# Optimization experiments

Hardware: AMD Instinct MI355X
Metric: run time of the kernel (lower is better)

The kernel has to match this reference:

```python
import jax, jax.numpy as jnp
import numpy as np

STATE_DIM = 4        # per-block state size (rel pos + rel vel, 2D)
N_NEIGH = 64         # neighbors per agent
BATCH = 4096         # observations in the batch (len(x) in torch code)
PHI_H, PHI_OUT = 256, 64
RHO_H, ACTION_DIM = 256, 2
R_AGENT = 0.15
A_MAX = 2.0


def setup_inputs() -> dict:
    key = jax.random.key(0)
    ks = jax.random.split(key, 5)

    def w(k, i, o):
        return jax.random.normal(k, (i, o), jnp.float32) / np.sqrt(i).astype(np.float32)

    x = jax.random.normal(ks[0], (BATCH, (N_NEIGH + 2) * STATE_DIM), jnp.float32)
    return dict(
        x=x,
        phi_w1=w(ks[1], STATE_DIM, PHI_H), phi_b1=jnp.zeros((PHI_H,), jnp.float32),
        phi_w2=w(ks[2], PHI_H, PHI_OUT), phi_b2=jnp.zeros((PHI_OUT,), jnp.float32),
        rho_w1=w(ks[3], PHI_OUT, RHO_H), rho_b1=jnp.zeros((RHO_H,), jnp.float32),
        rho_w2=w(ks[4], RHO_H, ACTION_DIM), rho_b2=jnp.zeros((ACTION_DIM,), jnp.float32),
    )


def reference(x, phi_w1, phi_b1, phi_w2, phi_b2, rho_w1, rho_b1, rho_w2, rho_b2):
    B = x.shape[0]
    blocks = x.reshape(B, -1, STATE_DIM)                 # [B, n_n+2, sd]
    # DeepSet: phi per block, permutation-invariant sum, rho head.
    h = jax.nn.relu(jnp.einsum('bns,sh->bnh', blocks, phi_w1) + phi_b1)
    phi = jnp.einsum('bnh,ho->bno', h, phi_w2) + phi_b2  # [B, n_n+2, phi_out]
    X = phi.sum(axis=1)                                  # [B, phi_out]
    h2 = jax.nn.relu(X @ rho_w1 + rho_b1)
    a = A_MAX * jnp.tanh(h2 @ rho_w2 + rho_b2)           # [B, action_dim]
    # Barrier: neighbor blocks start at block index 2; take first half (positions).
    p = blocks[:, 2:, : STATE_DIM // 2]                  # [B, n_n, 2]
    d = jnp.linalg.norm(p, axis=-1, keepdims=True)       # [B, n_n, 1]
    barrier = jnp.sum(-p / (d - R_AGENT) ** 2, axis=1)   # [B, 2]
    barrier = jax.lax.stop_gradient(barrier)  # torch goes through numpy -> detached
    a = a + barrier
    scale = A_MAX / jnp.max(a)  # torch.max(a_max)/torch.max(a_wbarrier), global max
    return jnp.where(scale < 1.0, a * scale, a)
```

## Files before the change

### kernel.cpp

```cpp
#include <hip/hip_runtime.h>
#include <math.h>


#define GROWS 4
#define NBLOCKS (4096 / GROWS)

__device__ __forceinline__ unsigned fkey(float f) {
    unsigned u = __float_as_uint(f);
    return (u & 0x80000000u) ? ~u : (u | 0x80000000u);
}
__device__ __forceinline__ float fkey_inv(unsigned k) {
    return __uint_as_float((k & 0x80000000u) ? (k & 0x7fffffffu) : ~k);
}
__device__ __forceinline__ float rlane(float v, int i) {
    return __uint_as_float(__builtin_amdgcn_readlane(__float_as_uint(v), i));
}

__global__ __launch_bounds__(256, 4) void barrier_net_main(
    const float* __restrict__ x,
    const float* __restrict__ w1,  const float* __restrict__ b1,
    const float* __restrict__ w2,  const float* __restrict__ b2,
    const float* __restrict__ rw1, const float* __restrict__ rb1,
    const float* __restrict__ rw2, const float* __restrict__ rb2,
    float* __restrict__ out, unsigned* __restrict__ maxkey)
{
    __shared__ float sH[GROWS][264];
    __shared__ float sXp[4][GROWS][68];
    __shared__ float sP4[4][GROWS][2];
    __shared__ float sbar[GROWS][2];
    __shared__ float sa[GROWS * 2];

    const int tid = threadIdx.x;
    const int ln  = tid & 63;
    const int wv  = tid >> 6;
    const int b0  = blockIdx.x * GROWS;
    const int row = __builtin_amdgcn_readfirstlane(b0 + wv);
    const float4* __restrict__ x4 = (const float4*)(x + (size_t)row * 264);

    float4 w1r0 = ((const float4*)(w1      ))[ln];
    float4 w1r1 = ((const float4*)(w1 + 256))[ln];
    float4 w1r2 = ((const float4*)(w1 + 512))[ln];
    float4 w1r3 = ((const float4*)(w1 + 768))[ln];
    float4 b1r  = ((const float4*)b1)[ln];
    float a0 = 0.f, a1 = 0.f, a2 = 0.f, a3 = 0.f;
    #pragma unroll 6
    for (int n = 0; n < 66; n++) {
        float4 xv = x4[n];
        float h0 = b1r.x, h1 = b1r.y, h2 = b1r.z, h3 = b1r.w;
        h0 = fmaf(xv.x, w1r0.x, h0); h1 = fmaf(xv.x, w1r0.y, h1);
        h2 = fmaf(xv.x, w1r0.z, h2); h3 = fmaf(xv.x, w1r0.w, h3);
        h0 = fmaf(xv.y, w1r1.x, h0); h1 = fmaf(xv.y, w1r1.y, h1);
        h2 = fmaf(xv.y, w1r1.z, h2); h3 = fmaf(xv.y, w1r1.w, h3);
        h0 = fmaf(xv.z, w1r2.x, h0); h1 = fmaf(xv.z, w1r2.y, h1);
        h2 = fmaf(xv.z, w1r2.z, h2); h3 = fmaf(xv.z, w1r2.w, h3);
        h0 = fmaf(xv.w, w1r3.x, h0); h1 = fmaf(xv.w, w1r3.y, h1);
        h2 = fmaf(xv.w, w1r3.z, h2); h3 = fmaf(xv.w, w1r3.w, h3);
        a0 += fmaxf(h0, 0.f); a1 += fmaxf(h1, 0.f);
        a2 += fmaxf(h2, 0.f); a3 += fmaxf(h3, 0.f);
    }
    ((float4*)sH[wv])[ln] = make_float4(a0, a1, a2, a3);

    {
        float4 pv = x4[ln + 2];
        float px = pv.x, py = pv.y;
        float d  = sqrtf(px * px + py * py);
        float t  = d - 0.15f;
        float inv = 1.0f / (t * t);
        float bx = -px * inv, by = -py * inv;
        #pragma unroll
        for (int m = 32; m >= 1; m >>= 1) {
            bx += __shfl_xor(bx, m);
            by += __shfl_xor(by, m);
        }
        if (ln == 0) { sbar[wv][0] = bx; sbar[wv][1] = by; }
    }
    __syncthreads();

    float Hq0 = sH[0][(wv << 6) + ln];
    float Hq1 = sH[1][(wv << 6) + ln];
    float Hq2 = sH[2][(wv << 6) + ln];
    float Hq3 = sH[3][(wv << 6) + ln];
    {
        float xp0 = 0.f, xp1 = 0.f, xp2 = 0.f, xp3 = 0.f;
        const float* w2q = w2 + (wv << 12);
        #pragma unroll 16
        for (int i = 0; i < 64; i++) {
            float wv2 = w2q[(i << 6) + ln];
            xp0 = fmaf(rlane(Hq0, i), wv2, xp0);
            xp1 = fmaf(rlane(Hq1, i), wv2, xp1);
            xp2 = fmaf(rlane(Hq2, i), wv2, xp2);
            xp3 = fmaf(rlane(Hq3, i), wv2, xp3);
        }
        sXp[wv][0][ln] = xp0; sXp[wv][1][ln] = xp1;
        sXp[wv][2][ln] = xp2; sXp[wv][3][ln] = xp3;
    }
    __syncthreads();

    float bb = 66.0f * b2[ln];
    float Xf0 = sXp[0][0][ln] + sXp[1][0][ln] + sXp[2][0][ln] + sXp[3][0][ln] + bb;
    float Xf1 = sXp[0][1][ln] + sXp[1][1][ln] + sXp[2][1][ln] + sXp[3][1][ln] + bb;
    float Xf2 = sXp[0][2][ln] + sXp[1][2][ln] + sXp[2][2][ln] + sXp[3][2][ln] + bb;
    float Xf3 = sXp[0][3][ln] + sXp[1][3][ln] + sXp[2][3][ln] + sXp[3][3][ln] + bb;

    float c0, c1, c2, c3;
    c0 = c1 = c2 = c3 = rb1[tid];
    #pragma unroll 16
    for (int i = 0; i < 64; i++) {
        float rwv = rw1[(i << 8) + tid];
        c0 = fmaf(rlane(Xf0, i), rwv, c0);
        c1 = fmaf(rlane(Xf1, i), rwv, c1);
        c2 = fmaf(rlane(Xf2, i), rwv, c2);
        c3 = fmaf(rlane(Xf3, i), rwv, c3);
    }
    c0 = fmaxf(c0, 0.f); c1 = fmaxf(c1, 0.f);
    c2 = fmaxf(c2, 0.f); c3 = fmaxf(c3, 0.f);

    {
        float2 r2 = ((const float2*)rw2)[tid];
        float p00 = c0 * r2.x, p01 = c0 * r2.y;
        float p10 = c1 * r2.x, p11 = c1 * r2.y;
        float p20 = c2 * r2.x, p21 = c2 * r2.y;
        float p30 = c3 * r2.x, p31 = c3 * r2.y;
        #pragma unroll
        for (int m = 32; m >= 1; m >>= 1) {
            p00 += __shfl_xor(p00, m); p01 += __shfl_xor(p01, m);
            p10 += __shfl_xor(p10, m); p11 += __shfl_xor(p11, m);
            p20 += __shfl_xor(p20, m); p21 += __shfl_xor(p21, m);
            p30 += __shfl_xor(p30, m); p31 += __shfl_xor(p31, m);
        }
        if (ln == 0) {
            sP4[wv][0][0] = p00; sP4[wv][0][1] = p01;
            sP4[wv][1][0] = p10; sP4[wv][1][1] = p11;
            sP4[wv][2][0] = p20; sP4[wv][2][1] = p21;
            sP4[wv][3][0] = p30; sP4[wv][3][1] = p31;
        }
    }
    __syncthreads();

    if (tid < GROWS * 2) {
        int r = tid >> 1, c = tid & 1;
        float pre = sP4[0][r][c] + sP4[1][r][c] + sP4[2][r][c] + sP4[3][r][c] + rb2[c];
        float a = 2.0f * tanhf(pre) + sbar[r][c];
        out[(b0 + r) * 2 + c] = a;
        sa[tid] = a;
    }
    __syncthreads();
    if (tid == 0) {
        float m = sa[0];
        #pragma unroll
        for (int i = 1; i < GROWS * 2; i++) m = fmaxf(m, sa[i]);
        atomicMax(maxkey, fkey(m));
    }
}

__global__ __launch_bounds__(256) void barrier_net_scale(
    float* __restrict__ out, const unsigned* __restrict__ maxkey)
{
    int i = blockIdx.x * 256 + threadIdx.x;
    float amax  = fkey_inv(*maxkey);
    float scale = 2.0f / amax;
    float a = out[i];
    out[i] = (scale < 1.0f) ? a * scale : a;
}

extern "C" void kernel_launch(void* const* d_in, const int* in_sizes, int n_in,
                              void* d_out, int out_size, void* d_ws, size_t ws_size,
                              hipStream_t stream) {
    const float* x   = (const float*)d_in[0];
    const float* w1  = (const float*)d_in[1];
    const float* b1  = (const float*)d_in[2];
    const float* w2  = (const float*)d_in[3];
    const float* b2  = (const float*)d_in[4];
    const float* rw1 = (const float*)d_in[5];
    const float* rb1 = (const float*)d_in[6];
    const float* rw2 = (const float*)d_in[7];
    const float* rb2 = (const float*)d_in[8];
    float* out = (float*)d_out;
    unsigned* maxkey = (unsigned*)d_ws;

    hipMemsetAsync(d_ws, 0, 4, stream);
    barrier_net_main<<<NBLOCKS, 256, 0, stream>>>(
        x, w1, b1, w2, b2, rw1, rb1, rw2, rb2, out, maxkey);
    barrier_net_scale<<<8192 / 256, 256, 0, stream>>>(out, maxkey);
}
```

Before: 98.68 us.

## Split fused DeepSet kernel into phase1 and phase234 with global H staging

Splits the single main kernel into two: the first computes the summed ReLU hidden activations and the barrier term per row and writes them to workspace, and the second runs the phi output layer and the rho MLP. The x row is now staged through shared memory instead of re-read per neighbor. The readlane broadcasts are replaced by float4 LDS reads. This trades an extra launch and a 4 MB global round-trip of H for simpler per-kernel register use and cheaper inner loops.

Result: slower. 104.1 us (+5.5%).

```diff
diff --git a/kernel.cpp b/kernel.cpp
--- a/kernel.cpp
+++ b/kernel.cpp
@@ -2,8 +2,7 @@
 #include <math.h>
 
 
-#define GROWS 4
-#define NBLOCKS (4096 / GROWS)
+#define NBLK 1024
 
 __device__ __forceinline__ unsigned fkey(float f) {
     unsigned u = __float_as_uint(f);
@@ -12,40 +11,35 @@
 __device__ __forceinline__ float fkey_inv(unsigned k) {
     return __uint_as_float((k & 0x80000000u) ? (k & 0x7fffffffu) : ~k);
 }
-__device__ __forceinline__ float rlane(float v, int i) {
-    return __uint_as_float(__builtin_amdgcn_readlane(__float_as_uint(v), i));
-}
-
-__global__ __launch_bounds__(256, 4) void barrier_net_main(
+
+__global__ __launch_bounds__(256, 4) void bn_phase1(
     const float* __restrict__ x,
-    const float* __restrict__ w1,  const float* __restrict__ b1,
-    const float* __restrict__ w2,  const float* __restrict__ b2,
-    const float* __restrict__ rw1, const float* __restrict__ rb1,
-    const float* __restrict__ rw2, const float* __restrict__ rb2,
-    float* __restrict__ out, unsigned* __restrict__ maxkey)
+    const float* __restrict__ w1, const float* __restrict__ b1,
+    float* __restrict__ H, float* __restrict__ bar)
 {
-    __shared__ float sH[GROWS][264];
-    __shared__ float sXp[4][GROWS][68];
-    __shared__ float sP4[4][GROWS][2];
-    __shared__ float sbar[GROWS][2];
-    __shared__ float sa[GROWS * 2];
+    __shared__ __align__(16) float sx[4][268];
 
     const int tid = threadIdx.x;
     const int ln  = tid & 63;
     const int wv  = tid >> 6;
-    const int b0  = blockIdx.x * GROWS;
-    const int row = __builtin_amdgcn_readfirstlane(b0 + wv);
+    const int row = blockIdx.x * 4 + wv;
     const float4* __restrict__ x4 = (const float4*)(x + (size_t)row * 264);
+
+    float4 xr = x4[ln];
+    float4 pv = x4[ln + 2];
+    ((float4*)sx[wv])[ln] = xr;
+    if (ln >= 62) ((float4*)sx[wv])[ln + 2] = pv;
 
     float4 w1r0 = ((const float4*)(w1      ))[ln];
     float4 w1r1 = ((const float4*)(w1 + 256))[ln];
     float4 w1r2 = ((const float4*)(w1 + 512))[ln];
     float4 w1r3 = ((const float4*)(w1 + 768))[ln];
     float4 b1r  = ((const float4*)b1)[ln];
+
     float a0 = 0.f, a1 = 0.f, a2 = 0.f, a3 = 0.f;
-    #pragma unroll 6
+    #pragma unroll 4
     for (int n = 0; n < 66; n++) {
-        float4 xv = x4[n];
+        float4 xv = ((const float4*)sx[wv])[n];
         float h0 = b1r.x, h1 = b1r.y, h2 = b1r.z, h3 = b1r.w;
         h0 = fmaf(xv.x, w1r0.x, h0); h1 = fmaf(xv.x, w1r0.y, h1);
         h2 = fmaf(xv.x, w1r0.z, h2); h3 = fmaf(xv.x, w1r0.w, h3);
@@ -58,10 +52,9 @@
         a0 += fmaxf(h0, 0.f); a1 += fmaxf(h1, 0.f);
         a2 += fmaxf(h2, 0.f); a3 += fmaxf(h3, 0.f);
     }
-    ((float4*)sH[wv])[ln] = make_float4(a0, a1, a2, a3);
-
-    {
-        float4 pv = x4[ln + 2];
+    ((float4*)(H + (size_t)row * 256))[ln] = make_float4(a0, a1, a2, a3);
+
+    {
         float px = pv.x, py = pv.y;
         float d  = sqrtf(px * px + py * py);
         float t  = d - 0.15f;
@@ -72,55 +65,96 @@
             bx += __shfl_xor(bx, m);
             by += __shfl_xor(by, m);
         }
-        if (ln == 0) { sbar[wv][0] = bx; sbar[wv][1] = by; }
-    }
-    __syncthreads();
-
-    float Hq0 = sH[0][(wv << 6) + ln];
-    float Hq1 = sH[1][(wv << 6) + ln];
-    float Hq2 = sH[2][(wv << 6) + ln];
-    float Hq3 = sH[3][(wv << 6) + ln];
+        if (ln == 0) { bar[row * 2 + 0] = bx; bar[row * 2 + 1] = by; }
+    }
+}
+
+__global__ __launch_bounds__(256, 4) void bn_phase234(
+    const float* __restrict__ H, const float* __restrict__ bar,
+    const float* __restrict__ w2,  const float* __restrict__ b2,
+    const float* __restrict__ rw1, const float* __restrict__ rb1,
+    const float* __restrict__ rw2, const float* __restrict__ rb2,
+    float* __restrict__ out, unsigned* __restrict__ wskey)
+{
+    __shared__ __align__(16) float sH[4][264];
+    __shared__ float sXp[4][4][68];
+    __shared__ __align__(16) float sX[4][68];
+    __shared__ float sP4[4][4][2];
+    __shared__ float sa[8];
+
+    const int tid = threadIdx.x;
+    const int ln  = tid & 63;
+    const int wv  = tid >> 6;
+    const int b0  = blockIdx.x * 4;
+
+    ((float4*)sH[wv])[ln] = ((const float4*)(H + (size_t)(b0 + wv) * 256))[ln];
+    __syncthreads();
+
     {
         float xp0 = 0.f, xp1 = 0.f, xp2 = 0.f, xp3 = 0.f;
         const float* w2q = w2 + (wv << 12);
-        #pragma unroll 16
-        for (int i = 0; i < 64; i++) {
-            float wv2 = w2q[(i << 6) + ln];
-            xp0 = fmaf(rlane(Hq0, i), wv2, xp0);
-            xp1 = fmaf(rlane(Hq1, i), wv2, xp1);
-            xp2 = fmaf(rlane(Hq2, i), wv2, xp2);
-            xp3 = fmaf(rlane(Hq3, i), wv2, xp3);
+        #pragma unroll 2
+        for (int i = 0; i < 16; i++) {
+            int kb = (wv << 4) + i;
+            float4 h0 = ((const float4*)sH[0])[kb];
+            float4 h1 = ((const float4*)sH[1])[kb];
+            float4 h2 = ((const float4*)sH[2])[kb];
+            float4 h3 = ((const float4*)sH[3])[kb];
+            float wk0 = w2q[((i << 2) + 0 << 6) + ln];
+            float wk1 = w2q[((i << 2) + 1 << 6) + ln];
+            float wk2 = w2q[((i << 2) + 2 << 6) + ln];
+            float wk3 = w2q[((i << 2) + 3 << 6) + ln];
+            xp0 = fmaf(h0.x, wk0, xp0); xp1 = fmaf(h1.x, wk0, xp1);
+            xp2 = fmaf(h2.x, wk0, xp2); xp3 = fmaf(h3.x, wk0, xp3);
+            xp0 = fmaf(h0.y, wk1, xp0); xp1 = fmaf(h1.y, wk1, xp1);
+            xp2 = fmaf(h2.y, wk1, xp2); xp3 = fmaf(h3.y, wk1, xp3);
+            xp0 = fmaf(h0.z, wk2, xp0); xp1 = fmaf(h1.z, wk2, xp1);
+            xp2 = fmaf(h2.z, wk2, xp2); xp3 = fmaf(h3.z, wk2, xp3);
+            xp0 = fmaf(h0.w, wk3, xp0); xp1 = fmaf(h1.w, wk3, xp1);
+            xp2 = fmaf(h2.w, wk3, xp2); xp3 = fmaf(h3.w, wk3, xp3);
         }
         sXp[wv][0][ln] = xp0; sXp[wv][1][ln] = xp1;
         sXp[wv][2][ln] = xp2; sXp[wv][3][ln] = xp3;
     }
     __syncthreads();
 
-    float bb = 66.0f * b2[ln];
-    float Xf0 = sXp[0][0][ln] + sXp[1][0][ln] + sXp[2][0][ln] + sXp[3][0][ln] + bb;
-    float Xf1 = sXp[0][1][ln] + sXp[1][1][ln] + sXp[2][1][ln] + sXp[3][1][ln] + bb;
-    float Xf2 = sXp[0][2][ln] + sXp[1][2][ln] + sXp[2][2][ln] + sXp[3][2][ln] + bb;
-    float Xf3 = sXp[0][3][ln] + sXp[1][3][ln] + sXp[2][3][ln] + sXp[3][3][ln] + bb;
+    {
+        float Xf = sXp[0][wv][ln] + sXp[1][wv][ln]
+                 + sXp[2][wv][ln] + sXp[3][wv][ln] + 66.0f * b2[ln];
+        sX[wv][ln] = Xf;
+    }
+    __syncthreads();
 
     float c0, c1, c2, c3;
     c0 = c1 = c2 = c3 = rb1[tid];
-    #pragma unroll 16
-    for (int i = 0; i < 64; i++) {
-        float rwv = rw1[(i << 8) + tid];
-        c0 = fmaf(rlane(Xf0, i), rwv, c0);
-        c1 = fmaf(rlane(Xf1, i), rwv, c1);
-        c2 = fmaf(rlane(Xf2, i), rwv, c2);
-        c3 = fmaf(rlane(Xf3, i), rwv, c3);
+    #pragma unroll 2
+    for (int i = 0; i < 16; i++) {
+        float4 X0 = ((const float4*)sX[0])[i];
+        float4 X1 = ((const float4*)sX[1])[i];
+        float4 X2 = ((const float4*)sX[2])[i];
+        float4 X3 = ((const float4*)sX[3])[i];
+        float r0 = rw1[((i << 2) + 0 << 8) + tid];
+        float r1 = rw1[((i << 2) + 1 << 8) + tid];
+        float r2 = rw1[((i << 2) + 2 << 8) + tid];
+        float r3 = rw1[((i << 2) + 3 << 8) + tid];
+        c0 = fmaf(X0.x, r0, c0); c1 = fmaf(X1.x, r0, c1);
+        c2 = fmaf(X2.x, r0, c2); c3 = fmaf(X3.x, r0, c3);
+        c0 = fmaf(X0.y, r1, c0); c1 = fmaf(X1.y, r1, c1);
+        c2 = fmaf(X2.y, r1, c2); c3 = fmaf(X3.y, r1, c3);
+        c0 = fmaf(X0.z, r2, c0); c1 = fmaf(X1.z, r2, c1);
+        c2 = fmaf(X2.z, r2, c2); c3 = fmaf(X3.z, r2, c3);
+        c0 = fmaf(X0.w, r3, c0); c1 = fmaf(X1.w, r3, c1);
+        c2 = fmaf(X2.w, r3, c2); c3 = fmaf(X3.w, r3, c3);
     }
     c0 = fmaxf(c0, 0.f); c1 = fmaxf(c1, 0.f);
     c2 = fmaxf(c2, 0.f); c3 = fmaxf(c3, 0.f);
 
     {
-        float2 r2 = ((const float2*)rw2)[tid];
-        float p00 = c0 * r2.x, p01 = c0 * r2.y;
-        float p10 = c1 * r2.x, p11 = c1 * r2.y;
-        float p20 = c2 * r2.x, p21 = c2 * r2.y;
-        float p30 = c3 * r2.x, p31 = c3 * r2.y;
+        float2 r2v = ((const float2*)rw2)[tid];
+        float p00 = c0 * r2v.x, p01 = c0 * r2v.y;
+        float p10 = c1 * r2v.x, p11 = c1 * r2v.y;
+        float p20 = c2 * r2v.x, p21 = c2 * r2v.y;
+        float p30 = c3 * r2v.x, p31 = c3 * r2v.y;
         #pragma unroll
         for (int m = 32; m >= 1; m >>= 1) {
             p00 += __shfl_xor(p00, m); p01 += __shfl_xor(p01, m);
@@ -137,27 +171,27 @@
     }
     __syncthreads();
 
-    if (tid < GROWS * 2) {
+    if (tid < 8) {
         int r = tid >> 1, c = tid & 1;
         float pre = sP4[0][r][c] + sP4[1][r][c] + sP4[2][r][c] + sP4[3][r][c] + rb2[c];
-        float a = 2.0f * tanhf(pre) + sbar[r][c];
-        out[(b0 + r) * 2 + c] = a;
+        float a = 2.0f * tanhf(pre) + bar[b0 * 2 + tid];
+        out[b0 * 2 + tid] = a;
         sa[tid] = a;
     }
     __syncthreads();
     if (tid == 0) {
         float m = sa[0];
         #pragma unroll
-        for (int i = 1; i < GROWS * 2; i++) m = fmaxf(m, sa[i]);
-        atomicMax(maxkey, fkey(m));
-    }
-}
-
-__global__ __launch_bounds__(256) void barrier_net_scale(
-    float* __restrict__ out, const unsigned* __restrict__ maxkey)
+        for (int i = 1; i < 8; i++) m = fmaxf(m, sa[i]);
+        atomicMax(wskey, fkey(m));
+    }
+}
+
+__global__ __launch_bounds__(256) void bn_scale(
+    float* __restrict__ out, const unsigned* __restrict__ wskey)
 {
     int i = blockIdx.x * 256 + threadIdx.x;
-    float amax  = fkey_inv(*maxkey);
+    float amax  = fkey_inv(*wskey);
     float scale = 2.0f / amax;
     float a = out[i];
     out[i] = (scale < 1.0f) ? a * scale : a;
@@ -176,10 +210,14 @@
     const float* rw2 = (const float*)d_in[7];
     const float* rb2 = (const float*)d_in[8];
     float* out = (float*)d_out;
-    unsigned* maxkey = (unsigned*)d_ws;
+
+    unsigned* wskey = (unsigned*)d_ws;
+    float* H   = (float*)((char*)d_ws + 1024);
+    float* bar = (float*)((char*)d_ws + 1024 + (size_t)4096 * 256 * 4);
 
     hipMemsetAsync(d_ws, 0, 4, stream);
-    barrier_net_main<<<NBLOCKS, 256, 0, stream>>>(
-        x, w1, b1, w2, b2, rw1, rb1, rw2, rb2, out, maxkey);
-    barrier_net_scale<<<8192 / 256, 256, 0, stream>>>(out, maxkey);
-}
+    bn_phase1<<<NBLK, 256, 0, stream>>>(x, w1, b1, H, bar);
+    bn_phase234<<<NBLK, 256, 0, stream>>>(H, bar, w2, b2, rw1, rb1, rw2, rb2,
+                                          out, wskey);
+    bn_scale<<<8192 / 256, 256, 0, stream>>>(out, wskey);
+}
```
